# Kernel optimization log

Measured on AMD Instinct MI355X. Metric: run time of the kernel, lower is better.

Reference implementation:

```python
import jax, jax.numpy as jnp
import numpy as np

B, N, HD = 2, 2048, 2048
NH, KVH = 16, 4
D = HD // NH          # 128
R = NH // KVH         # 4 (kv_ratio)
KVD = KVH * D         # 512


def setup_inputs() -> dict:
    key = jax.random.key(0)
    ks = jax.random.split(key, 6)
    s = 0.02
    return {
        "tokens": jax.random.normal(ks[0], (B, N, HD), jnp.float32),
        "norm_w": jnp.ones((HD,), jnp.float32),
        "Wq": jax.random.normal(ks[1], (HD, HD), jnp.float32) * s,
        "bq": jnp.zeros((HD,), jnp.float32),
        "Wk": jax.random.normal(ks[2], (KVD, HD), jnp.float32) * s,
        "bk": jnp.zeros((KVD,), jnp.float32),
        "Wv": jax.random.normal(ks[3], (KVD, HD), jnp.float32) * s,
        "bv": jnp.zeros((KVD,), jnp.float32),
        "Wo": jax.random.normal(ks[4], (HD, HD), jnp.float32) * s,
        "bo": jnp.zeros((HD,), jnp.float32),
    }


def reference(tokens, norm_w, Wq, bq, Wk, bk, Wv, bv, Wo, bo):
    # RMSNorm (torch default eps=None -> finfo eps), learnable weight
    eps = jnp.finfo(tokens.dtype).eps
    x = tokens * jax.lax.rsqrt(jnp.mean(tokens * tokens, axis=-1, keepdims=True) + eps) * norm_w

    # projections -> [B, heads, N, D]
    q = (x @ Wq.T + bq).reshape(B, N, NH, D).transpose(0, 2, 1, 3)
    k = (x @ Wk.T + bk).reshape(B, N, KVH, D).transpose(0, 2, 1, 3)
    v = (x @ Wv.T + bv).reshape(B, N, KVH, D).transpose(0, 2, 1, 3)

    # GQA via tiling the kv block (matches torch.cat of copies: head h uses kv head h % KVH)
    k = jnp.tile(k, (1, R, 1, 1))
    v = jnp.tile(v, (1, R, 1, 1))

    # Faithful (inverted) mask: True where j <= i, and True positions are masked out.
    mask = jnp.arange(N)[None, :] <= jnp.arange(N)[:, None]  # [N, N]

    # No 1/sqrt(D) scaling in the original
    scores = jnp.einsum('bhid,bhjd->bhij', q, k)
    scores = jnp.where(mask[None, None, :, :], jnp.float32(-1e9), scores)
    attn = jax.nn.softmax(scores, axis=-1)

    a = jnp.einsum('bhij,bhjd->bhid', attn, v)       # [B, NH, N, D]
    a = a.transpose(0, 2, 1, 3).reshape(B, N, HD)    # [B, N, HD]
    return a @ Wo.T + bo
```

## Files before the change

### kernel.cpp

```cpp
#include <hip/hip_runtime.h>

#define BB   2
#define NN   2048
#define HDIM 2048
#define NHD  16
#define KVHD 4
#define DD   128
#define KVW  1024
#define MTOK (BB*NN)
#define NSPLIT 7

typedef _Float16 h8 __attribute__((ext_vector_type(8)));
typedef _Float16 h4 __attribute__((ext_vector_type(4)));
typedef float    f4 __attribute__((ext_vector_type(4)));
typedef float    fx16 __attribute__((ext_vector_type(16)));
typedef short    b8 __attribute__((ext_vector_type(8)));
typedef unsigned int u4v __attribute__((ext_vector_type(4)));

static __device__ __forceinline__ f4 mfma16(h8 a, h8 b, f4 c) {
    return __builtin_amdgcn_mfma_f32_16x16x32_f16(a, b, c, 0, 0, 0);
}
static __device__ __forceinline__ fx16 mfma32b(b8 a, b8 b, fx16 c) {
    return __builtin_amdgcn_mfma_f32_32x32x16_bf16(a, b, c, 0, 0, 0);
}

static __device__ __forceinline__ unsigned short f2bf(float f) {
    unsigned int u = __float_as_uint(f);
    u += 0x7FFF + ((u >> 16) & 1);
    return (unsigned short)(u >> 16);
}

static __device__ __forceinline__ void gload_lds16(const void* g, void* l) {
    __builtin_amdgcn_global_load_lds(
        (const __attribute__((address_space(1))) void*)g,
        (__attribute__((address_space(3))) void*)l, 16, 0, 0);
}

__global__ __launch_bounds__(256) void rmsnorm_k(const float* __restrict__ t,
                                                 const float* __restrict__ wn,
                                                 _Float16* __restrict__ xh) {
    const int row = blockIdx.x, tid = threadIdx.x;
    const float* rp = t + (size_t)row * HDIM;
    float4 v[2];
    float ss = 0.f;
    #pragma unroll
    for (int p = 0; p < 2; ++p) {
        float4 x = *(const float4*)(rp + (p * 256 + tid) * 4);
        v[p] = x;
        ss += x.x * x.x + x.y * x.y + x.z * x.z + x.w * x.w;
    }
    #pragma unroll
    for (int off = 32; off; off >>= 1) ss += __shfl_xor(ss, off, 64);
    __shared__ float sred[4];
    if ((tid & 63) == 0) sred[tid >> 6] = ss;
    __syncthreads();
    float rs = rsqrtf((sred[0] + sred[1] + sred[2] + sred[3]) * (1.0f / HDIM)
                      + 1.1920928955078125e-07f);
    _Float16* op = xh + (size_t)row * HDIM;
    #pragma unroll
    for (int p = 0; p < 2; ++p) {
        int base = (p * 256 + tid) * 4;
        float4 w = *(const float4*)(wn + base);
        h4 o;
        o[0] = (_Float16)(v[p].x * rs * w.x);
        o[1] = (_Float16)(v[p].y * rs * w.y);
        o[2] = (_Float16)(v[p].z * rs * w.z);
        o[3] = (_Float16)(v[p].w * rs * w.w);
        *(h4*)(op + base) = o;
    }
}

__global__ __launch_bounds__(256) void cvtall_k(const float* __restrict__ Wq,
                                                const float* __restrict__ Wk,
                                                const float* __restrict__ Wv,
                                                const float* __restrict__ Wo,
                                                _Float16* __restrict__ wq_h,
                                                _Float16* __restrict__ wkv_h,
                                                _Float16* __restrict__ wo_h) {
    int blk = blockIdx.x;
    const float* src; _Float16* dst; int off;
    if (blk < 4096)      { src = Wq; dst = wq_h;               off = blk; }
    else if (blk < 5120) { src = Wk; dst = wkv_h;              off = blk - 4096; }
    else if (blk < 6144) { src = Wv; dst = wkv_h + 512 * HDIM; off = blk - 5120; }
    else                 { src = Wo; dst = wo_h;               off = blk - 6144; }
    int i = off * 1024 + threadIdx.x * 4;
    float4 v = *(const float4*)(src + i);
    h4 o; o[0] = (_Float16)v.x; o[1] = (_Float16)v.y;
    o[2] = (_Float16)v.z; o[3] = (_Float16)v.w;
    *(h4*)(dst + i) = o;
}

__global__ void biascat_k(const float* __restrict__ bq, const float* __restrict__ bk,
                          const float* __restrict__ bv,
                          float* __restrict__ bqkv, float* __restrict__ vsum) {
    int i = blockIdx.x * 256 + threadIdx.x;
    bqkv[i] = (i < 2048) ? bq[i] : (i < 2560) ? bk[i - 2048] : bv[i - 2560];
    if (i < 1024) vsum[i] = 0.f;
}

__global__ __launch_bounds__(256) void vtrans_k(const _Float16* __restrict__ kv,
                                                unsigned short* __restrict__ vt) {
    const int tid = threadIdx.x;
    const int tok = blockIdx.x * 64 + (tid & 63);
    const int kvh = blockIdx.y;
    const int d0 = (tid >> 6) * 32;
    const int b = tok >> 11, n = tok & (NN - 1);
    const _Float16* src = kv + (size_t)tok * KVW + 512 + kvh * DD + d0;
    unsigned short* dstb = vt + ((size_t)(b * KVHD + kvh) * DD) * NN + n;
    #pragma unroll
    for (int u = 0; u < 4; ++u) {
        h8 v = *(const h8*)(src + u * 8);
        #pragma unroll
        for (int e = 0; e < 8; ++e)
            dstb[(size_t)(d0 + u * 8 + e) * NN] = f2bf((float)v[e]);
    }
}

template <int MODE>
__global__ __launch_bounds__(256, 2) void gemm_bt(const _Float16* __restrict__ A,
                                                  const _Float16* __restrict__ Bw,
                                                  const float* __restrict__ bias,
                                                  void* __restrict__ Cout,
                                                  void* __restrict__ Cout2,
                                                  int Ndim, int K) {
    __shared__ _Float16 sA[128 * 64];
    __shared__ _Float16 sB[128 * 64];
    const int tid = threadIdx.x;
    const int lane = tid & 63, w = tid >> 6;
    const int ln = lane & 15, quad = lane >> 4;
    const int wm = w >> 1, wn = w & 1;
    const int m0 = blockIdx.y * 128, n0 = blockIdx.x * 128;

    f4 acc[4][4] = {};
    for (int k0 = 0; k0 < K; k0 += 64) {
        #pragma unroll
        for (int it = 0; it < 4; ++it) {
            int chunk = it * 256 + tid;
            int row = chunk >> 3, p = chunk & 7;
            int c = p ^ (row & 7);
            gload_lds16(A + (size_t)(m0 + row) * K + k0 + c * 8, sA + chunk * 8);
            gload_lds16(Bw + (size_t)(n0 + row) * K + k0 + c * 8, sB + chunk * 8);
        }
        __syncthreads();
        #pragma unroll
        for (int kk = 0; kk < 2; ++kk) {
            h8 af[4], bf[4];
            #pragma unroll
            for (int mt = 0; mt < 4; ++mt)
                af[mt] = *(const h8*)&sA[(wm * 64 + mt * 16 + ln) * 64 +
                                         (((kk * 4 + quad) ^ (ln & 7)) << 3)];
            #pragma unroll
            for (int nt = 0; nt < 4; ++nt)
                bf[nt] = *(const h8*)&sB[(wn * 64 + nt * 16 + ln) * 64 +
                                         (((kk * 4 + quad) ^ (ln & 7)) << 3)];
            #pragma unroll
            for (int mt = 0; mt < 4; ++mt)
                #pragma unroll
                for (int nt = 0; nt < 4; ++nt)
                    acc[mt][nt] = mfma16(af[mt], bf[nt], acc[mt][nt]);
        }
        __syncthreads();
    }
    #pragma unroll
    for (int mt = 0; mt < 4; ++mt) {
        int rowb = m0 + wm * 64 + mt * 16 + quad * 4;
        #pragma unroll
        for (int nt = 0; nt < 4; ++nt) {
            int col = n0 + wn * 64 + nt * 16 + ln;
            float bv = bias[col];
            #pragma unroll
            for (int r = 0; r < 4; ++r) {
                float v = acc[mt][nt][r] + bv;
                if (MODE == 1)
                    ((float*)Cout)[(size_t)(rowb + r) * Ndim + col] = v;
                else {
                    if (n0 < 2048)
                        ((_Float16*)Cout)[(size_t)(rowb + r) * HDIM + col] = (_Float16)v;
                    else
                        ((_Float16*)Cout2)[(size_t)(rowb + r) * KVW + (col - 2048)] = (_Float16)v;
                }
            }
        }
    }
}

__device__ __constant__ int piece_tab[23] = {
    7,
    0x10000, 0x10100,
    8,
    0x10001, 0x10101,
    0x10002, 0x10102,
    9,
    0x10003, 0x10103,
    0x10004, 0x10104,
    10,
    0x10005, 0x10105,
    0x10006, 0x10106,
    11, 12, 13, 14, 15
};

__global__ __launch_bounds__(256, 2) void attn_k(const _Float16* __restrict__ qh,
                                                 const _Float16* __restrict__ kvp,
                                                 const unsigned short* __restrict__ vt,
                                                 _Float16* __restrict__ ah,
                                                 float* __restrict__ O_ws,
                                                 float* __restrict__ l_ws) {
    __shared__ _Float16 s_k[2][64 * 128];
    __shared__ unsigned short s_v[2][128 * 64];
    const int tid = threadIdx.x;
    const int lane = tid & 63, w = tid >> 6;
    const int ln = lane & 15, quad = lane >> 4;
    const int l5 = lane & 31, hi = lane >> 5;
    const int sel = quad & 1;
    const int idx = blockIdx.x;
    const int hb = idx & 31;
    const int h = hb & 15, b = hb >> 4;
    const int code = piece_tab[idx >> 5];
    const int x = code & 255, p = (code >> 8) & 1;
    const bool is_split = (code >> 16) & 1;
    int jlo, jhi;
    if (is_split) { int len = 16 - x; jlo = 2 * x + p * len; jhi = jlo + len; }
    else          { jlo = 2 * x; jhi = 32; }
    const int i0 = x * 128;
    const int kvh = h & 3;

    h8 qf[2][4];
    #pragma unroll
    for (int t = 0; t < 2; ++t) {
        const _Float16* qrow =
            qh + ((size_t)(b * NN + i0 + w * 32 + t * 16 + ln)) * HDIM + h * DD;
        #pragma unroll
        for (int kc = 0; kc < 4; ++kc)
            qf[t][kc] = *(const h8*)(qrow + kc * 32 + quad * 8);
    }

    b8 ones;
    #pragma unroll
    for (int e = 0; e < 8; ++e) ones[e] = (short)0x3F80;

    fx16 O[4] = {};
    fx16 OS = {};

    auto stage = [&](int jt, int bufi) {
        const int j0s = jt * 64;
        #pragma unroll
        for (int itr = 0; itr < 4; ++itr) {
            int chunk = itr * 256 + tid;
            int jj = chunk >> 4, pp = chunk & 15;
            int c = pp ^ (jj & 15);
            gload_lds16(kvp + ((size_t)(b * NN + j0s + jj)) * KVW + kvh * DD + c * 8,
                        &s_k[bufi][chunk * 8]);
        }
        #pragma unroll
        for (int itr = 0; itr < 4; ++itr) {
            int chunk = itr * 256 + tid;
            int d = chunk >> 3, pp = chunk & 7;
            int c = pp ^ (d & 7);
            gload_lds16(vt + ((size_t)(b * KVHD + kvh) * DD + d) * NN + j0s + c * 8,
                        &s_v[bufi][chunk * 8]);
        }
    };

    stage(jlo, 0);
    for (int jt = jlo; jt < jhi; ++jt) {
        const int j0 = jt * 64;
        const int cur = (jt - jlo) & 1;
        __syncthreads();
        if (jt + 1 < jhi) stage(jt + 1, cur ^ 1);

        f4 sc[2][4] = {};
        #pragma unroll
        for (int nt = 0; nt < 4; ++nt)
            #pragma unroll
            for (int kc = 0; kc < 4; ++kc) {
                h8 kf = *(const h8*)&s_k[cur][(nt * 16 + ln) * 128 +
                                              (((kc * 4 + quad) ^ ln) << 3)];
                sc[0][nt] = mfma16(kf, qf[0][kc], sc[0][nt]);
                sc[1][nt] = mfma16(kf, qf[1][kc], sc[1][nt]);
            }

        const bool need_mask = (jt < 2 * x + 2);
        unsigned int u0[4][2], u1[4][2];
        #pragma unroll
        for (int nt = 0; nt < 4; ++nt)
            #pragma unroll
            for (int rr = 0; rr < 2; ++rr) {
                float a0 = sc[0][nt][2 * rr], a1 = sc[0][nt][2 * rr + 1];
                float c0 = sc[1][nt][2 * rr], c1 = sc[1][nt][2 * rr + 1];
                if (need_mask) {
                    int jg = j0 + nt * 16 + quad * 4 + 2 * rr;
                    int ig0 = i0 + w * 32 + ln;
                    int ig1 = ig0 + 16;
                    if (jg <= ig0) a0 = -1e9f;
                    if (jg + 1 <= ig0) a1 = -1e9f;
                    if (jg <= ig1) c0 = -1e9f;
                    if (jg + 1 <= ig1) c1 = -1e9f;
                }
                u0[nt][rr] = (unsigned int)f2bf(__expf(a0)) |
                             ((unsigned int)f2bf(__expf(a1)) << 16);
                u1[nt][rr] = (unsigned int)f2bf(__expf(c0)) |
                             ((unsigned int)f2bf(__expf(c1)) << 16);
            }

        b8 paf[4];
        #pragma unroll
        for (int nt = 0; nt < 4; ++nt) {
            unsigned int own0 = sel ? u1[nt][0] : u0[nt][0];
            unsigned int own1 = sel ? u1[nt][1] : u0[nt][1];
            unsigned int oth0 = sel ? u0[nt][0] : u1[nt][0];
            unsigned int oth1 = sel ? u0[nt][1] : u1[nt][1];
            unsigned int r0 = __shfl_xor(oth0, 16, 64);
            unsigned int r1 = __shfl_xor(oth1, 16, 64);
            u4v pw;
            pw[0] = sel ? r0 : own0;
            pw[1] = sel ? r1 : own1;
            pw[2] = sel ? own0 : r0;
            pw[3] = sel ? own1 : r1;
            paf[nt] = __builtin_bit_cast(b8, pw);
        }

        #pragma unroll
        for (int nt = 0; nt < 4; ++nt) {
            #pragma unroll
            for (int dblk = 0; dblk < 4; ++dblk) {
                b8 bv = *(const b8*)&s_v[cur][(dblk * 32 + l5) * 64 +
                                              (((nt * 2 + hi) ^ (l5 & 7)) << 3)];
                O[dblk] = mfma32b(paf[nt], bv, O[dblk]);
            }
            OS = mfma32b(paf[nt], ones, OS);
        }
    }

    if (is_split) {
        size_t po = (((size_t)(b * NHD + h) * NSPLIT + x) * 2 + p);
        float* Op = O_ws + po * 16384;
        float* Lp = l_ws + po * 128;
        #pragma unroll
        for (int nt4 = 0; nt4 < 4; ++nt4)
            #pragma unroll
            for (int rg = 0; rg < 16; ++rg) {
                int q = (rg & 3) + 8 * (rg >> 2) + 4 * hi;
                Op[(w * 32 + q) * 128 + nt4 * 32 + l5] = O[nt4][rg];
            }
        if (l5 == 0) {
            #pragma unroll
            for (int rg = 0; rg < 16; ++rg) {
                int q = (rg & 3) + 8 * (rg >> 2) + 4 * hi;
                Lp[w * 32 + q] = OS[rg];
            }
        }
    } else {
        float inv_l[16];
        #pragma unroll
        for (int rg = 0; rg < 16; ++rg) inv_l[rg] = 1.0f / OS[rg];
        #pragma unroll
        for (int nt4 = 0; nt4 < 4; ++nt4)
            #pragma unroll
            for (int rg = 0; rg < 16; ++rg) {
                int q = (rg & 3) + 8 * (rg >> 2) + 4 * hi;
                ah[((size_t)(b * NN + i0 + w * 32 + q)) * HDIM + h * DD + nt4 * 32 + l5] =
                    (_Float16)(O[nt4][rg] * inv_l[rg]);
            }
    }
}

__global__ __launch_bounds__(256) void combine_k(const float* __restrict__ O_ws,
                                                 const float* __restrict__ l_ws,
                                                 _Float16* __restrict__ ah) {
    const int x = blockIdx.x, h = blockIdx.y, b = blockIdx.z;
    const int tid = threadIdx.x;
    const int d = tid & 127;
    size_t po = (((size_t)(b * NHD + h) * NSPLIT + x) * 2);
    const float* O0 = O_ws + po * 16384;
    const float* O1 = O0 + 16384;
    const float* L0 = l_ws + po * 128;
    const float* L1 = L0 + 128;
    for (int ql = tid >> 7; ql < 128; ql += 2) {
        float l = L0[ql] + L1[ql];
        float o = O0[ql * 128 + d] + O1[ql * 128 + d];
        ah[((size_t)(b * NN + x * 128 + ql)) * HDIM + h * DD + d] = (_Float16)(o / l);
    }
}

__global__ __launch_bounds__(256) void vsum_k(const _Float16* __restrict__ kvp,
                                              float* __restrict__ vsum) {
    __shared__ float red[16][128];
    const int seg = blockIdx.x, kvh = blockIdx.y, b = blockIdx.z;
    const int tid = threadIdx.x;
    const int jj = tid >> 4, dc = (tid & 15) * 8;
    float acc[8] = {};
    #pragma unroll 4
    for (int j = seg * 256 + jj; j < seg * 256 + 256; j += 16) {
        h8 v = *(const h8*)(kvp + ((size_t)(b * NN + j)) * KVW + 512 + kvh * DD + dc);
        #pragma unroll
        for (int e = 0; e < 8; ++e) acc[e] += (float)v[e];
    }
    #pragma unroll
    for (int e = 0; e < 8; ++e) red[jj][dc + e] = acc[e];
    __syncthreads();
    if (tid < 128) {
        float s = 0.f;
        #pragma unroll
        for (int t = 0; t < 16; ++t) s += red[t][tid];
        atomicAdd(&vsum[(b * KVHD + kvh) * DD + tid], s);
    }
}

__global__ void fixup_write_k(const float* __restrict__ vsum,
                              _Float16* __restrict__ ah) {
    int b = blockIdx.x >> 2, kvh = blockIdx.x & 3, d = threadIdx.x;
    float mean = vsum[(b * KVHD + kvh) * DD + d] * (1.0f / NN);
    #pragma unroll
    for (int r = 0; r < 4; ++r) {
        int h = r * 4 + kvh;
        ah[((size_t)(b * NN + NN - 1)) * HDIM + h * DD + d] = (_Float16)mean;
    }
}

extern "C" void kernel_launch(void* const* d_in, const int* in_sizes, int n_in,
                              void* d_out, int out_size, void* d_ws, size_t ws_size,
                              hipStream_t stream) {
    const float* tokens = (const float*)d_in[0];
    const float* norm_w = (const float*)d_in[1];
    const float* Wq = (const float*)d_in[2];
    const float* bq = (const float*)d_in[3];
    const float* Wk = (const float*)d_in[4];
    const float* bk = (const float*)d_in[5];
    const float* Wv = (const float*)d_in[6];
    const float* bv = (const float*)d_in[7];
    const float* Wo = (const float*)d_in[8];
    const float* bo = (const float*)d_in[9];
    float* out = (float*)d_out;

    char* ws = (char*)d_ws;
    _Float16* x_h   = (_Float16*)(ws);
    _Float16* wq_h  = (_Float16*)(ws + 16777216);
    _Float16* wkv_h = (_Float16*)(ws + 25165824);
    _Float16* wo_h  = (_Float16*)(ws + 29360128);
    _Float16* q_h   = (_Float16*)(ws + 37752832);
    _Float16* kv_h  = (_Float16*)(ws + 54530048);
    _Float16* a_h   = (_Float16*)(ws + 62918656);
    unsigned short* vt_h = (unsigned short*)(ws + 79695872);
    float*    vsum  = (float*)   (ws + 83890176);
    float*    l_ws  = (float*)   (ws + 83894272);
    float*    bqkv  = (float*)   (ws + 84123648);
    float*    O_ws  = (float*)(ws);

    rmsnorm_k<<<MTOK, 256, 0, stream>>>(tokens, norm_w, x_h);
    cvtall_k<<<10240, 256, 0, stream>>>(Wq, Wk, Wv, Wo, wq_h, wkv_h, wo_h);
    biascat_k<<<12, 256, 0, stream>>>(bq, bk, bv, bqkv, vsum);

    gemm_bt<2><<<dim3(3072 / 128, MTOK / 128), 256, 0, stream>>>(
        x_h, wq_h, bqkv, (void*)q_h, (void*)kv_h, 3072, HDIM);

    vtrans_k<<<dim3(MTOK / 64, KVHD), 256, 0, stream>>>(kv_h, vt_h);

    attn_k<<<736, 256, 0, stream>>>(q_h, kv_h, vt_h, a_h, O_ws, l_ws);
    combine_k<<<dim3(NSPLIT, NHD, BB), 256, 0, stream>>>(O_ws, l_ws, a_h);
    vsum_k<<<dim3(8, KVHD, BB), 256, 0, stream>>>(kv_h, vsum);
    fixup_write_k<<<BB * KVHD, 128, 0, stream>>>(vsum, a_h);

    gemm_bt<1><<<dim3(HDIM / 128, MTOK / 128), 256, 0, stream>>>(
        a_h, wo_h, bo, (void*)out, nullptr, HDIM, HDIM);
}
```

Baseline: 313.9 us.

## Use 32x32 MFMA for QK scores and permute V layout to drop shuffles

Result: no change. 316.6 us (+0.9%).

```diff
diff --git a/kernel.cpp b/kernel.cpp
--- a/kernel.cpp
+++ b/kernel.cpp
@@ -17,6 +17,9 @@
 typedef short    b8 __attribute__((ext_vector_type(8)));
 typedef unsigned int u4v __attribute__((ext_vector_type(4)));
 
+static __device__ __forceinline__ fx16 mfma32h(h8 a, h8 b, fx16 c) {
+    return __builtin_amdgcn_mfma_f32_32x32x16_f16(a, b, c, 0, 0, 0);
+}
 static __device__ __forceinline__ f4 mfma16(h8 a, h8 b, f4 c) {
     return __builtin_amdgcn_mfma_f32_16x16x32_f16(a, b, c, 0, 0, 0);
 }
@@ -105,8 +108,9 @@
     const int kvh = blockIdx.y;
     const int d0 = (tid >> 6) * 32;
     const int b = tok >> 11, n = tok & (NN - 1);
+    const int n2 = (n & ~12) | ((n & 4) << 1) | ((n & 8) >> 1);
     const _Float16* src = kv + (size_t)tok * KVW + 512 + kvh * DD + d0;
-    unsigned short* dstb = vt + ((size_t)(b * KVHD + kvh) * DD) * NN + n;
+    unsigned short* dstb = vt + ((size_t)(b * KVHD + kvh) * DD) * NN + n2;
     #pragma unroll
     for (int u = 0; u < 4; ++u) {
         h8 v = *(const h8*)(src + u * 8);
@@ -209,9 +213,7 @@
     __shared__ unsigned short s_v[2][128 * 64];
     const int tid = threadIdx.x;
     const int lane = tid & 63, w = tid >> 6;
-    const int ln = lane & 15, quad = lane >> 4;
     const int l5 = lane & 31, hi = lane >> 5;
-    const int sel = quad & 1;
     const int idx = blockIdx.x;
     const int hb = idx & 31;
     const int h = hb & 15, b = hb >> 4;
@@ -223,15 +225,15 @@
     else          { jlo = 2 * x; jhi = 32; }
     const int i0 = x * 128;
     const int kvh = h & 3;
-
-    h8 qf[2][4];
-    #pragma unroll
-    for (int t = 0; t < 2; ++t) {
+    const int qg = i0 + w * 32 + l5;
+
+    h8 qf[8];
+    {
         const _Float16* qrow =
-            qh + ((size_t)(b * NN + i0 + w * 32 + t * 16 + ln)) * HDIM + h * DD;
-        #pragma unroll
-        for (int kc = 0; kc < 4; ++kc)
-            qf[t][kc] = *(const h8*)(qrow + kc * 32 + quad * 8);
+            qh + ((size_t)(b * NN + qg)) * HDIM + h * DD;
+        #pragma unroll
+        for (int kc = 0; kc < 8; ++kc)
+            qf[kc] = *(const h8*)(qrow + kc * 16 + hi * 8);
     }
 
     b8 ones;
@@ -268,66 +270,49 @@
         __syncthreads();
         if (jt + 1 < jhi) stage(jt + 1, cur ^ 1);
 
-        f4 sc[2][4] = {};
-        #pragma unroll
-        for (int nt = 0; nt < 4; ++nt)
-            #pragma unroll
-            for (int kc = 0; kc < 4; ++kc) {
-                h8 kf = *(const h8*)&s_k[cur][(nt * 16 + ln) * 128 +
-                                              (((kc * 4 + quad) ^ ln) << 3)];
-                sc[0][nt] = mfma16(kf, qf[0][kc], sc[0][nt]);
-                sc[1][nt] = mfma16(kf, qf[1][kc], sc[1][nt]);
-            }
+        fx16 sc0 = {}, sc1 = {};
+        #pragma unroll
+        for (int kc = 0; kc < 8; ++kc) {
+            int cs = ((kc * 2 + hi) ^ (l5 & 15)) << 3;
+            h8 k0 = *(const h8*)&s_k[cur][l5 * 128 + cs];
+            h8 k1 = *(const h8*)&s_k[cur][(32 + l5) * 128 + cs];
+            sc0 = mfma32h(k0, qf[kc], sc0);
+            sc1 = mfma32h(k1, qf[kc], sc1);
+        }
 
         const bool need_mask = (jt < 2 * x + 2);
-        unsigned int u0[4][2], u1[4][2];
-        #pragma unroll
-        for (int nt = 0; nt < 4; ++nt)
-            #pragma unroll
-            for (int rr = 0; rr < 2; ++rr) {
-                float a0 = sc[0][nt][2 * rr], a1 = sc[0][nt][2 * rr + 1];
-                float c0 = sc[1][nt][2 * rr], c1 = sc[1][nt][2 * rr + 1];
+        #pragma unroll
+        for (int jb = 0; jb < 2; ++jb) {
+            const fx16& sc = jb ? sc1 : sc0;
+            unsigned int pwod[8];
+            #pragma unroll
+            for (int pr = 0; pr < 8; ++pr) {
+                float s0 = sc[2 * pr], s1 = sc[2 * pr + 1];
                 if (need_mask) {
-                    int jg = j0 + nt * 16 + quad * 4 + 2 * rr;
-                    int ig0 = i0 + w * 32 + ln;
-                    int ig1 = ig0 + 16;
-                    if (jg <= ig0) a0 = -1e9f;
-                    if (jg + 1 <= ig0) a1 = -1e9f;
-                    if (jg <= ig1) c0 = -1e9f;
-                    if (jg + 1 <= ig1) c1 = -1e9f;
+                    int rg0 = 2 * pr;
+                    int jg0 = j0 + jb * 32 + (rg0 & 3) + 8 * (rg0 >> 2) + 4 * hi;
+                    if (jg0 <= qg) s0 = -1e9f;
+                    if (jg0 + 1 <= qg) s1 = -1e9f;
                 }
-                u0[nt][rr] = (unsigned int)f2bf(__expf(a0)) |
-                             ((unsigned int)f2bf(__expf(a1)) << 16);
-                u1[nt][rr] = (unsigned int)f2bf(__expf(c0)) |
-                             ((unsigned int)f2bf(__expf(c1)) << 16);
-            }
-
-        b8 paf[4];
-        #pragma unroll
-        for (int nt = 0; nt < 4; ++nt) {
-            unsigned int own0 = sel ? u1[nt][0] : u0[nt][0];
-            unsigned int own1 = sel ? u1[nt][1] : u0[nt][1];
-            unsigned int oth0 = sel ? u0[nt][0] : u1[nt][0];
-            unsigned int oth1 = sel ? u0[nt][1] : u1[nt][1];
-            unsigned int r0 = __shfl_xor(oth0, 16, 64);
-            unsigned int r1 = __shfl_xor(oth1, 16, 64);
-            u4v pw;
-            pw[0] = sel ? r0 : own0;
-            pw[1] = sel ? r1 : own1;
-            pw[2] = sel ? own0 : r0;
-            pw[3] = sel ? own1 : r1;
-            paf[nt] = __builtin_bit_cast(b8, pw);
-        }
-
-        #pragma unroll
-        for (int nt = 0; nt < 4; ++nt) {
-            #pragma unroll
-            for (int dblk = 0; dblk < 4; ++dblk) {
-                b8 bv = *(const b8*)&s_v[cur][(dblk * 32 + l5) * 64 +
-                                              (((nt * 2 + hi) ^ (l5 & 7)) << 3)];
-                O[dblk] = mfma32b(paf[nt], bv, O[dblk]);
-            }
-            OS = mfma32b(paf[nt], ones, OS);
+                pwod[pr] = (unsigned int)f2bf(__expf(s0)) |
+                           ((unsigned int)f2bf(__expf(s1)) << 16);
+            }
+            u4v w0v = {pwod[0], pwod[1], pwod[2], pwod[3]};
+            u4v w1v = {pwod[4], pwod[5], pwod[6], pwod[7]};
+            b8 pa0 = __builtin_bit_cast(b8, w0v);
+            b8 pa1 = __builtin_bit_cast(b8, w1v);
+
+            #pragma unroll
+            for (int ks = 0; ks < 2; ++ks) {
+                b8 pa = ks ? pa1 : pa0;
+                #pragma unroll
+                for (int dblk = 0; dblk < 4; ++dblk) {
+                    b8 bv = *(const b8*)&s_v[cur][(dblk * 32 + l5) * 64 +
+                                                  (((jb * 4 + ks * 2 + hi) ^ (l5 & 7)) << 3)];
+                    O[dblk] = mfma32b(pa, bv, O[dblk]);
+                }
+                OS = mfma32b(pa, ones, OS);
+            }
         }
     }
 
```
